# Optimization experiments

Hardware: AMD Instinct MI355X
Metric: run time of the kernel (lower is better)

## Reference

```python
import jax, jax.numpy as jnp
import numpy as np

K_ORDER = 3  # spline order k from init_kwargs


def get_spline_basis(x_ext, grid, k):
    # x_ext: (n, batch), grid: (n, G+2k+1)
    grid = grid[:, :, None]          # (n, P, 1)
    x = x_ext[:, None, :]            # (n, 1, batch)
    # order-0 indicator bases
    bases = ((x >= grid[:, :-1]) & (x < grid[:, 1:])).astype(x_ext.dtype)
    # Cox-de Boor recursion up to order k
    for K in range(1, k + 1):
        left = (x - grid[:, :-(K + 1)]) / (grid[:, K:-1] - grid[:, :-(K + 1)])
        right = (grid[:, K + 1:] - x) / (grid[:, K + 1:] - grid[:, 1:-K])
        bases = left * bases[:, :-1] + right * bases[:, 1:]
    return bases  # (n, G+k, batch)


def setup_inputs() -> dict:
    key = jax.random.key(0)
    k1, k2 = jax.random.split(key)
    n_in, n_out, batch, k = 64, 64, 2048, K_ORDER
    n = n_in * n_out
    init_G = 3
    h = 2.0 / init_G  # (1 - (-1)) / init_G
    grid_row = jnp.arange(-k, init_G + k + 1, dtype=jnp.float32) * h - 1.0  # (G+2k+1,) = (10,)
    grid = jnp.tile(grid_row[None, :], (n, 1))                              # (n, 10)
    x = jax.random.normal(k1, (batch, n_in), dtype=jnp.float32)
    c_basis = 0.1 * jax.random.normal(k2, (n, init_G + k), dtype=jnp.float32)  # (n, 6)
    c_spl = jnp.ones((n,), dtype=jnp.float32)
    c_res = jnp.ones((n,), dtype=jnp.float32)
    return {"x": x, "c_basis": c_basis, "c_spl": c_spl, "c_res": c_res, "grid": grid}


def reference(x, c_basis, c_spl, c_res, grid):
    batch, n_in = x.shape
    n = grid.shape[0]
    n_out = n // n_in
    # replicate each input across n_out outgoing edges: flat index = out*n_in + in
    x_ext = jnp.broadcast_to(x[:, None, :], (batch, n_out, n_in)).reshape(batch, n).T  # (n, batch)
    # residual branch: swish
    res = (x_ext * jax.nn.sigmoid(x_ext)).T  # (batch, n)
    # spline branch
    Bi = get_spline_basis(x_ext, grid, K_ORDER)        # (n, G+k, batch)
    spl = jnp.einsum('ij,ijk->ki', c_basis, Bi)        # (batch, n)
    y = c_spl[None, :] * spl + c_res[None, :] * res    # (batch, n)
    y = y.reshape(batch, n_out, n_in).sum(axis=2) / n_in  # (batch, n_out)
    # spline regularization term
    grid_r = grid.reshape(n_out, n_in, -1)
    input_norm = grid_r[:, :, -1] - grid_r[:, :, 0] + 1e-05
    spl_reg = jnp.mean(jnp.abs(spl.reshape(batch, n_out, n_in)), axis=0) / input_norm  # (n_out, n_in)
    return (y, spl_reg)
```

## Files before the change

kernel.cpp:

```cpp
#include <hip/hip_runtime.h>
#include <math.h>


#define BATCHN 2048
#define NI     64
#define NO     64
#define NTOTAL 4096
#define BB     8
#define NCHUNK (BATCHN / BB)
#define TPB    512

__device__ __forceinline__ void eval_basis6(float xv,
                                            const float* tt,
                                            const float* inv1,
                                            const float* inv2,
                                            const float* inv3,
                                            float* bout, float* silu)
{
    float c[10], d[10];
#pragma unroll
    for (int m = 0; m < 10; ++m) {
        c[m] = (xv >= tt[m]) ? 1.0f : 0.0f;
        d[m] = xv - tt[m];
    }
    float b[9], w[9];
#pragma unroll
    for (int m = 0; m < 9; ++m) b[m] = c[m] - c[m + 1];
#pragma unroll
    for (int m = 0; m < 9; ++m) w[m] = b[m] * inv1[m];
#pragma unroll
    for (int m = 0; m < 8; ++m) b[m] = d[m] * w[m] - d[m + 2] * w[m + 1];
#pragma unroll
    for (int m = 0; m < 8; ++m) w[m] = b[m] * inv2[m];
#pragma unroll
    for (int m = 0; m < 7; ++m) b[m] = d[m] * w[m] - d[m + 3] * w[m + 1];
#pragma unroll
    for (int m = 0; m < 7; ++m) w[m] = b[m] * inv3[m];
#pragma unroll
    for (int m = 0; m < 6; ++m) bout[m] = d[m] * w[m] - d[m + 4] * w[m + 1];
    *silu = xv / (1.0f + expf(-xv));
}

__global__ __launch_bounds__(TPB, 2) void kan_main(
    const float* __restrict__ x, const float* __restrict__ cb,
    const float* __restrict__ c_spl, const float* __restrict__ c_res,
    const float* __restrict__ grid, float* __restrict__ y,
    float* __restrict__ regpart, int write_part)
{
    __shared__ float sB[7][512];
    const int t    = threadIdx.x;
    const int lane = t & 63;
    const int wv   = t >> 6;
    const int bchunk = blockIdx.x;
    const int bbase  = bchunk * BB;

    float tt[10];
#pragma unroll
    for (int m = 0; m < 10; ++m) tt[m] = grid[m];
    float inv1[9], inv2[8], inv3[7];
#pragma unroll
    for (int m = 0; m < 9; ++m) inv1[m] = 1.0f / (tt[m + 1] - tt[m]);
#pragma unroll
    for (int m = 0; m < 8; ++m) inv2[m] = 1.0f / (tt[m + 2] - tt[m]);
#pragma unroll
    for (int m = 0; m < 7; ++m) inv3[m] = 1.0f / (tt[m + 3] - tt[m]);

    {
        const float xv = x[bbase * NI + t];
        float bo[6], sl;
        eval_basis6(xv, tt, inv1, inv2, inv3, bo, &sl);
#pragma unroll
        for (int m = 0; m < 6; ++m) sB[m][t] = bo[m];
        sB[6][t] = sl;
    }
    __syncthreads();

    float B0[8], B1[8], B2[8], B3[8], B4[8], B5[8], SL[8];
#pragma unroll
    for (int bb = 0; bb < 8; ++bb) {
        const int p = bb * 64 + lane;
        B0[bb] = sB[0][p]; B1[bb] = sB[1][p]; B2[bb] = sB[2][p];
        B3[bb] = sB[3][p]; B4[bb] = sB[4][p]; B5[bb] = sB[5][p];
        SL[bb] = sB[6][p];
    }

    const bool p0 = (lane & 1), p1 = (lane & 2), p2 = (lane & 4);
#pragma unroll
    for (int jj = 0; jj < 8; ++jj) {
        const int j = jj * TPB + t;
        const float* cbp = cb + j * 6;
        const float2 c01 = *(const float2*)(cbp);
        const float2 c23 = *(const float2*)(cbp + 2);
        const float2 c45 = *(const float2*)(cbp + 4);
        const float cs = c_spl[j];
        const float cr = c_res[j];

        float v[8];
        float rabs = 0.0f;
#pragma unroll
        for (int bb = 0; bb < 8; ++bb) {
            float s = c01.x * B0[bb];
            s = fmaf(c01.y, B1[bb], s);
            s = fmaf(c23.x, B2[bb], s);
            s = fmaf(c23.y, B3[bb], s);
            s = fmaf(c45.x, B4[bb], s);
            s = fmaf(c45.y, B5[bb], s);
            rabs += fabsf(s);
            v[bb] = fmaf(cs, s, cr * SL[bb]);
        }
        if (write_part) regpart[bchunk * NTOTAL + j] = rabs;

#pragma unroll
        for (int r = 0; r < 4; ++r) {
            float send = p0 ? v[r] : v[r + 4];
            float recv = __shfl_xor(send, 1, 64);
            float keep = p0 ? v[r + 4] : v[r];
            v[r] = keep + recv;
        }
#pragma unroll
        for (int r = 0; r < 2; ++r) {
            float send = p1 ? v[r] : v[r + 2];
            float recv = __shfl_xor(send, 2, 64);
            float keep = p1 ? v[r + 2] : v[r];
            v[r] = keep + recv;
        }
        {
            float send = p2 ? v[0] : v[1];
            float recv = __shfl_xor(send, 4, 64);
            float keep = p2 ? v[1] : v[0];
            v[0] = keep + recv;
        }
        v[0] += __shfl_xor(v[0], 8, 64);
        v[0] += __shfl_xor(v[0], 16, 64);
        v[0] += __shfl_xor(v[0], 32, 64);
        if (lane < 8) {
            const int bbL = ((lane & 1) << 2) | (lane & 2) | ((lane >> 2) & 1);
            const int o = jj * 8 + wv;
            y[(bbase + bbL) * NO + o] = v[0] * (1.0f / 64.0f);
        }
    }
}

__global__ __launch_bounds__(256) void kan_reduce(
    const float* __restrict__ regpart, const float* __restrict__ grid,
    float* __restrict__ outreg)
{
    __shared__ float sR[4][64];
    const int t = threadIdx.x;
    const int qo = t & 63, gs = t >> 6;
    const int q = blockIdx.x * 64 + qo;
    float s = 0.0f;
#pragma unroll 16
    for (int g = gs * 64; g < gs * 64 + 64; ++g) s += regpart[g * NTOTAL + q];
    sR[gs][qo] = s;
    __syncthreads();
    if (t < 64) {
        const float tot = sR[0][qo] + sR[1][qo] + sR[2][qo] + sR[3][qo];
        const float norm = grid[q * 10 + 9] - grid[q * 10] + 1e-5f;
        outreg[q] = (tot * (1.0f / (float)BATCHN)) / norm;
    }
}

__global__ __launch_bounds__(256) void kan_reg_standalone(
    const float* __restrict__ x, const float* __restrict__ cb,
    const float* __restrict__ grid, float* __restrict__ outreg)
{
    __shared__ float sB2[6][256];
    __shared__ float sR[256];
    const int t = threadIdx.x;
    const int i = blockIdx.x;

    float tt[10];
#pragma unroll
    for (int m = 0; m < 10; ++m) tt[m] = grid[m];
    float inv1[9], inv2[8], inv3[7];
#pragma unroll
    for (int m = 0; m < 9; ++m) inv1[m] = 1.0f / (tt[m + 1] - tt[m]);
#pragma unroll
    for (int m = 0; m < 8; ++m) inv2[m] = 1.0f / (tt[m + 2] - tt[m]);
#pragma unroll
    for (int m = 0; m < 7; ++m) inv3[m] = 1.0f / (tt[m + 3] - tt[m]);

    const int o = t >> 2;
    const int q = t & 3;
    const int j = o * NI + i;
    const float c0 = cb[j * 6 + 0], c1 = cb[j * 6 + 1], c2 = cb[j * 6 + 2];
    const float c3 = cb[j * 6 + 3], c4 = cb[j * 6 + 4], c5 = cb[j * 6 + 5];

    float acc = 0.0f;
    for (int tile = 0; tile < 8; ++tile) {
        const float xv = x[(tile * 256 + t) * NI + i];
        float bo[6], sl;
        eval_basis6(xv, tt, inv1, inv2, inv3, bo, &sl);
        __syncthreads();
#pragma unroll
        for (int m = 0; m < 6; ++m) sB2[m][t] = bo[m];
        __syncthreads();
        for (int bi = 0; bi < 64; ++bi) {
            const int b = q * 64 + ((bi + q * 8) & 63);
            float s = c0 * sB2[0][b];
            s = fmaf(c1, sB2[1][b], s);
            s = fmaf(c2, sB2[2][b], s);
            s = fmaf(c3, sB2[3][b], s);
            s = fmaf(c4, sB2[4][b], s);
            s = fmaf(c5, sB2[5][b], s);
            acc += fabsf(s);
        }
    }
    sR[t] = acc;
    __syncthreads();
    if (t < 64) {
        const float s = sR[t * 4 + 0] + sR[t * 4 + 1] + sR[t * 4 + 2] + sR[t * 4 + 3];
        const int jj = t * NI + i;
        const float norm = grid[jj * 10 + 9] - grid[jj * 10] + 1e-5f;
        outreg[jj] = (s * (1.0f / (float)BATCHN)) / norm;
    }
}

extern "C" void kernel_launch(void* const* d_in, const int* in_sizes, int n_in,
                              void* d_out, int out_size, void* d_ws, size_t ws_size,
                              hipStream_t stream) {
    (void)in_sizes; (void)n_in; (void)out_size;
    const float* x    = (const float*)d_in[0];
    const float* cb   = (const float*)d_in[1];
    const float* cspl = (const float*)d_in[2];
    const float* cres = (const float*)d_in[3];
    const float* grid = (const float*)d_in[4];
    float* y      = (float*)d_out;
    float* outreg = y + BATCHN * NO;

    const size_t needed = (size_t)NCHUNK * NTOTAL * sizeof(float);
    if (ws_size >= needed) {
        float* part = (float*)d_ws;
        kan_main<<<NCHUNK, TPB, 0, stream>>>(x, cb, cspl, cres, grid, y, part, 1);
        kan_reduce<<<NTOTAL / 64, 256, 0, stream>>>(part, grid, outreg);
    } else {
        kan_main<<<NCHUNK, TPB, 0, stream>>>(x, cb, cspl, cres, grid, y,
                                             (float*)d_ws, 0);
        kan_reg_standalone<<<NI, 256, 0, stream>>>(x, cb, grid, outreg);
    }
}
```

Measured before the change: 74.18 us.

## Split main kernel across output halves, stage y in LDS, widen reduce grid

Measured after the change: 72.75 us. About the same (-1.9%).

```diff
diff --git a/kernel.cpp b/kernel.cpp
--- a/kernel.cpp
+++ b/kernel.cpp
@@ -41,17 +41,19 @@
     *silu = xv / (1.0f + expf(-xv));
 }
 
-__global__ __launch_bounds__(TPB, 2) void kan_main(
+__global__ __launch_bounds__(TPB, 4) void kan_main(
     const float* __restrict__ x, const float* __restrict__ cb,
     const float* __restrict__ c_spl, const float* __restrict__ c_res,
     const float* __restrict__ grid, float* __restrict__ y,
     float* __restrict__ regpart, int write_part)
 {
-    __shared__ float sB[7][512];
+    __shared__ float4 sB4[2][TPB];
+    __shared__ float  sY[8][33];
     const int t    = threadIdx.x;
     const int lane = t & 63;
     const int wv   = t >> 6;
-    const int bchunk = blockIdx.x;
+    const int bchunk = blockIdx.x >> 1;
+    const int half   = blockIdx.x & 1;
     const int bbase  = bchunk * BB;
 
     float tt[10];
@@ -69,9 +71,8 @@
         const float xv = x[bbase * NI + t];
         float bo[6], sl;
         eval_basis6(xv, tt, inv1, inv2, inv3, bo, &sl);
-#pragma unroll
-        for (int m = 0; m < 6; ++m) sB[m][t] = bo[m];
-        sB[6][t] = sl;
+        sB4[0][t] = make_float4(bo[0], bo[1], bo[2], bo[3]);
+        sB4[1][t] = make_float4(bo[4], bo[5], sl, 0.0f);
     }
     __syncthreads();
 
@@ -79,15 +80,17 @@
 #pragma unroll
     for (int bb = 0; bb < 8; ++bb) {
         const int p = bb * 64 + lane;
-        B0[bb] = sB[0][p]; B1[bb] = sB[1][p]; B2[bb] = sB[2][p];
-        B3[bb] = sB[3][p]; B4[bb] = sB[4][p]; B5[bb] = sB[5][p];
-        SL[bb] = sB[6][p];
+        const float4 a = sB4[0][p];
+        const float4 b = sB4[1][p];
+        B0[bb] = a.x; B1[bb] = a.y; B2[bb] = a.z; B3[bb] = a.w;
+        B4[bb] = b.x; B5[bb] = b.y; SL[bb] = b.z;
     }
 
     const bool p0 = (lane & 1), p1 = (lane & 2), p2 = (lane & 4);
-#pragma unroll
-    for (int jj = 0; jj < 8; ++jj) {
-        const int j = jj * TPB + t;
+#pragma unroll 2
+    for (int jj4 = 0; jj4 < 4; ++jj4) {
+        const int jj = (half << 2) + jj4;
+        const int j  = jj * TPB + t;
         const float* cbp = cb + j * 6;
         const float2 c01 = *(const float2*)(cbp);
         const float2 c23 = *(const float2*)(cbp + 2);
@@ -135,9 +138,14 @@
         v[0] += __shfl_xor(v[0], 32, 64);
         if (lane < 8) {
             const int bbL = ((lane & 1) << 2) | (lane & 2) | ((lane >> 2) & 1);
-            const int o = jj * 8 + wv;
-            y[(bbase + bbL) * NO + o] = v[0] * (1.0f / 64.0f);
-        }
+            sY[bbL][(jj4 << 3) + wv] = v[0] * (1.0f / 64.0f);
+        }
+    }
+    __syncthreads();
+
+    if (t < 256) {
+        const int bbL = t >> 5, oo = t & 31;
+        y[(bbase + bbL) * NO + (half << 5) + oo] = sY[bbL][oo];
     }
 }
 
@@ -145,19 +153,22 @@
     const float* __restrict__ regpart, const float* __restrict__ grid,
     float* __restrict__ outreg)
 {
-    __shared__ float sR[4][64];
-    const int t = threadIdx.x;
-    const int qo = t & 63, gs = t >> 6;
-    const int q = blockIdx.x * 64 + qo;
+    __shared__ float sR[16][17];
+    const int t  = threadIdx.x;
+    const int qo = t & 15, gs = t >> 4;
+    const int q  = blockIdx.x * 16 + qo;
     float s = 0.0f;
-#pragma unroll 16
-    for (int g = gs * 64; g < gs * 64 + 64; ++g) s += regpart[g * NTOTAL + q];
+#pragma unroll
+    for (int g = gs * 16; g < gs * 16 + 16; ++g) s += regpart[g * NTOTAL + q];
     sR[gs][qo] = s;
     __syncthreads();
-    if (t < 64) {
-        const float tot = sR[0][qo] + sR[1][qo] + sR[2][qo] + sR[3][qo];
-        const float norm = grid[q * 10 + 9] - grid[q * 10] + 1e-5f;
-        outreg[q] = (tot * (1.0f / (float)BATCHN)) / norm;
+    if (t < 16) {
+        float tot = 0.0f;
+#pragma unroll
+        for (int g2 = 0; g2 < 16; ++g2) tot += sR[g2][t];
+        const int jq = blockIdx.x * 16 + t;
+        const float norm = grid[jq * 10 + 9] - grid[jq * 10] + 1e-5f;
+        outreg[jq] = (tot * (1.0f / (float)BATCHN)) / norm;
     }
 }
 
@@ -232,11 +243,11 @@
     const size_t needed = (size_t)NCHUNK * NTOTAL * sizeof(float);
     if (ws_size >= needed) {
         float* part = (float*)d_ws;
-        kan_main<<<NCHUNK, TPB, 0, stream>>>(x, cb, cspl, cres, grid, y, part, 1);
-        kan_reduce<<<NTOTAL / 64, 256, 0, stream>>>(part, grid, outreg);
+        kan_main<<<NCHUNK * 2, TPB, 0, stream>>>(x, cb, cspl, cres, grid, y, part, 1);
+        kan_reduce<<<NTOTAL / 16, 256, 0, stream>>>(part, grid, outreg);
     } else {
-        kan_main<<<NCHUNK, TPB, 0, stream>>>(x, cb, cspl, cres, grid, y,
-                                             (float*)d_ws, 0);
+        kan_main<<<NCHUNK * 2, TPB, 0, stream>>>(x, cb, cspl, cres, grid, y,
+                                                 (float*)d_ws, 0);
         kan_reg_standalone<<<NI, 256, 0, stream>>>(x, cb, grid, outreg);
     }
 }
```
